# Kernel tuning notes

Measured on AMD Instinct MI355X. Metric: run time of the kernel, lower is better.

The kernel has to match this reference:

```python
import jax, jax.numpy as jnp
import numpy as np

BN_EPS = 1e-5

def binary_activation(x):
    # ReActNet BinaryActivation: forward = sign(x), backward = piecewise poly STE
    out_fwd = jnp.sign(x)
    m1 = (x < -1.0).astype(x.dtype)
    m2 = (x < 0.0).astype(x.dtype)
    m3 = (x < 1.0).astype(x.dtype)
    out1 = -1.0 * m1 + (x * x + 2.0 * x) * (1.0 - m1)
    out2 = out1 * m2 + (-x * x + 2.0 * x) * (1.0 - m2)
    out3 = out2 * m3 + 1.0 * (1.0 - m3)
    return jax.lax.stop_gradient(out_fwd - out3) + out3

def binary_conv3x3(x, w, stride=1):
    # per-output-channel scaling = mean |w| over (in, kh, kw), detached
    scale = jax.lax.stop_gradient(jnp.mean(jnp.abs(w), axis=(1, 2, 3), keepdims=True))
    bw_no_grad = jax.lax.stop_gradient(scale * jnp.sign(w))
    cw = jnp.clip(w, -1.0, 1.0)
    bw = bw_no_grad - jax.lax.stop_gradient(cw) + cw
    return jax.lax.conv_general_dilated(
        x, bw, window_strides=(stride, stride), padding=[(1, 1), (1, 1)],
        dimension_numbers=('NCHW', 'OIHW', 'NCHW'))

def batchnorm_inference(y, gamma, beta, mean, var):
    inv = gamma * jax.lax.rsqrt(var + BN_EPS)
    return y * inv[None, :, None, None] + (beta - mean * inv)[None, :, None, None]

def setup_inputs() -> dict:
    key = jax.random.key(0)
    k1, k2, k3 = jax.random.split(key, 3)
    N, Cin, Cout, H, W = 64, 128, 128, 56, 56
    x = jax.random.normal(k1, (N, Cin, H, W), dtype=jnp.float32)
    weight = jax.random.normal(k2, (Cout, Cin, 3, 3), dtype=jnp.float32) * 0.1
    gamma = jnp.ones((Cout,), dtype=jnp.float32)
    beta = jnp.zeros((Cout,), dtype=jnp.float32)
    bn_mean = jnp.zeros((Cout,), dtype=jnp.float32)
    bn_var = jax.random.uniform(k3, (Cout,), dtype=jnp.float32)
    return {"x": x, "weight": weight, "gamma": gamma, "beta": beta,
            "bn_mean": bn_mean, "bn_var": bn_var}

def reference(x, weight, gamma, beta, bn_mean, bn_var):
    residual = x
    out = binary_activation(x)
    out = binary_conv3x3(out, weight, stride=1)
    out = batchnorm_inference(out, gamma, beta, bn_mean, bn_var)
    return out + residual
```

## Files before the change

kernel.cpp:

```cpp
#include <hip/hip_runtime.h>


#define N_   64
#define C_   128
#define H_   56
#define W_   56
#define HW_  (H_*W_)
#define PH_  (H_+2)
#define PW_  (W_+2)
#define PHW_ (PH_*PW_)
#define NPIX (N_*HW_)
#define NPAD (N_*PHW_)
#define SBYTES ((size_t)NPAD * 128)
#define SPIX 264

typedef int v4i  __attribute__((ext_vector_type(4)));
typedef int v16i __attribute__((ext_vector_type(16)));

__device__ __forceinline__ void glds16(const char* g, char* l) {
    __builtin_amdgcn_global_load_lds(
        (const __attribute__((address_space(1))) void*)g,
        (__attribute__((address_space(3))) void*)l, 16, 0, 0);
}

__device__ __forceinline__ unsigned sign_byte(unsigned u) {
    return ((u << 1) == 0u) ? 0u : ((u >> 31) ? 0xFFu : 1u);
}

__global__ void prep_w_kernel(const float* __restrict__ w,
                              const float* __restrict__ gamma,
                              const float* __restrict__ beta,
                              const float* __restrict__ bn_mean,
                              const float* __restrict__ bn_var,
                              v4i* __restrict__ wfrag,
                              float2* __restrict__ AB) {
    const int o = blockIdx.x;
    const int lane = threadIdx.x;
    const float* wo = w + o * 1152;

    float s = 0.f;
    #pragma unroll
    for (int k = 0; k < 18; k++) s += fabsf(wo[k * 64 + lane]);
    #pragma unroll
    for (int off = 32; off > 0; off >>= 1) s += __shfl_down(s, off);

    #pragma unroll
    for (int rep = 0; rep < 2; rep++) {
        int f = rep * 64 + lane;
        if (f < 72) {
            int t = f >> 3, ks = (f >> 1) & 3, lh = f & 1;
            int cbase = ks * 32 + lh * 16;
            unsigned d[4];
            #pragma unroll
            for (int i = 0; i < 4; i++) {
                unsigned wd = 0;
                #pragma unroll
                for (int j = 0; j < 4; j++) {
                    unsigned u = __float_as_uint(wo[(cbase + i * 4 + j) * 9 + t]);
                    wd |= sign_byte(u) << (8 * j);
                }
                d[i] = wd;
            }
            v4i v; v.x=(int)d[0]; v.y=(int)d[1]; v.z=(int)d[2]; v.w=(int)d[3];
            wfrag[(((o >> 5) * 9 + t) * 4 + ks) * 64 + (lh << 5) + (o & 31)] = v;
        }
    }
    if (lane == 0) {
        float scale = s * (1.0f / 1152.0f);
        float inv = gamma[o] * rsqrtf(bn_var[o] + 1e-5f);
        float2 ab; ab.x = scale * inv; ab.y = beta[o] - bn_mean[o] * inv;
        AB[o] = ab;
    }
}

__global__ __launch_bounds__(256) void pack_s_kernel(
        const float* __restrict__ x, char* __restrict__ S) {
    const int tid = threadIdx.x;
    const int pixl = tid & 63, q = tid >> 6;
    const int b = blockIdx.x;

    if (b >= NPIX / 64) {
        int bt = (b - NPIX / 64) * 64 + pixl;
        int n = bt / 228, e = bt - n * 228;
        int ph, pw;
        if (e < 58)       { ph = 0;  pw = e; }
        else if (e < 116) { ph = 57; pw = e - 58; }
        else { int i = e - 116; ph = 1 + (i >> 1); pw = (i & 1) ? 57 : 0; }
        v4i z = {};
        char* dst = S + (size_t)((n * PH_ + ph) * PW_ + pw) * 128 + q * 32;
        ((v4i*)dst)[0] = z;
        ((v4i*)dst)[1] = z;
        return;
    }

    const int g = b * 64 + pixl;
    const int n = g / HW_;
    const int p = g - n * HW_;
    const int row = p / W_, col = p - row * W_;

    const float* xp = x + ((size_t)n * C_ + q * 32) * HW_ + p;
    unsigned w[8];
    #pragma unroll
    for (int i = 0; i < 8; i++) {
        unsigned wd = 0;
        #pragma unroll
        for (int j = 0; j < 4; j++) {
            unsigned u = __float_as_uint(xp[(i * 4 + j) * HW_]);
            wd |= sign_byte(u) << (8 * j);
        }
        w[i] = wd;
    }
    const int P = (n * PH_ + row + 1) * PW_ + col + 1;
    const int m = P & 7;
    char* base = S + (size_t)P * 128;
    v4i t0; t0.x=(int)w[0]; t0.y=(int)w[1]; t0.z=(int)w[2]; t0.w=(int)w[3];
    v4i t1; t1.x=(int)w[4]; t1.y=(int)w[5]; t1.z=(int)w[6]; t1.w=(int)w[7];
    *(v4i*)(base + (((2 * q)     ^ m) << 4)) = t0;
    *(v4i*)(base + (((2 * q + 1) ^ m) << 4)) = t1;
}

__global__ __launch_bounds__(256, 3) void bconv_mfma_kernel(
        const char* __restrict__ S,
        const v4i* __restrict__ wfrag,
        const float2* __restrict__ AB,
        const float* __restrict__ x,
        float* __restrict__ out) {
    __shared__ char Sl[SPIX * 128];

    const int tid = threadIdx.x;
    const int lane = tid & 63;
    const int wid = tid >> 6;
    const int l31 = lane & 31, lhi = lane >> 5;

    const int b0 = blockIdx.x;
    const int bid = (b0 & 7) * 200 + (b0 >> 3);
    const int n = bid / 25;
    const int pb = bid - n * 25;
    const int p0 = pb * 128;

    const int r0 = p0 / W_, c0 = p0 - r0 * W_;
    const int P0 = (n * PH_ + r0 + 1) * PW_ + (c0 + 1);
    const int qs8 = (P0 - PW_ - 1) & ~7;

    {
        const char* gsrc = S + (size_t)qs8 * 128 + lane * 16;
        #pragma unroll
        for (int i = 0; i < 9; i++) {
            int seg = i * 4 + wid;
            if (seg < (SPIX * 128) / 1024)
                glds16(gsrc + seg * 1024, &Sl[seg * 1024]);
        }
    }

    int lpx[4]; bool val[4]; int pix[4];
    #pragma unroll
    for (int ch = 0; ch < 4; ch++) {
        int p = p0 + ch * 32 + l31;
        val[ch] = (p < HW_);
        if (!val[ch]) p = HW_ - 1;
        pix[ch] = p;
        int r = p / W_, c = p - r * W_;
        lpx[ch] = (n * PH_ + r + 1) * PW_ + (c + 1) - qs8;
    }
    const int kc1 = lhi << 4;

    __syncthreads();

    v16i acc[4] = {};
    const v4i* wbase = wfrag + (size_t)wid * (9 * 4 * 64) + lane;

    v4i Acur[4], Anxt[4];
    #pragma unroll
    for (int ks = 0; ks < 4; ks++) Acur[ks] = wbase[ks * 64];

    #pragma unroll
    for (int t = 0; t < 9; t++) {
        if (t < 8) {
            #pragma unroll
            for (int ks = 0; ks < 4; ks++)
                Anxt[ks] = wbase[((t + 1) * 4 + ks) * 64];
        }
        const int tp = (t / 3 - 1) * PW_ + (t % 3 - 1);
        int A0[4];
        #pragma unroll
        for (int ch = 0; ch < 4; ch++) {
            int lpt = lpx[ch] + tp;
            A0[ch] = (lpt << 7) ^ ((lpt & 7) << 4) ^ kc1;
        }
        #pragma unroll
        for (int ks = 0; ks < 4; ks++) {
            #pragma unroll
            for (int ch = 0; ch < 4; ch++) {
                v4i bb = *(const v4i*)(&Sl[A0[ch] ^ (ks << 5)]);
                acc[ch] = __builtin_amdgcn_mfma_i32_32x32x32_i8(Acur[ks], bb,
                                                                acc[ch], 0, 0, 0);
            }
        }
        if (t < 8) {
            #pragma unroll
            for (int ks = 0; ks < 4; ks++) Acur[ks] = Anxt[ks];
        }
    }

    const int obase = wid * 32 + 4 * lhi;
    #pragma unroll
    for (int ch = 0; ch < 4; ch++) {
        if (!val[ch]) continue;
        unsigned base = (unsigned)n * (unsigned)(C_ * HW_) + (unsigned)pix[ch];
        #pragma unroll
        for (int r = 0; r < 16; r++) {
            int o = obase + (r & 3) + 8 * (r >> 2);
            float2 ab = AB[o];
            unsigned idx = base + (unsigned)o * (unsigned)HW_;
            out[idx] = fmaf(ab.x, (float)acc[ch][r], ab.y) + x[idx];
        }
    }
}

extern "C" void kernel_launch(void* const* d_in, const int* in_sizes, int n_in,
                              void* d_out, int out_size, void* d_ws, size_t ws_size,
                              hipStream_t stream) {
    const float* x      = (const float*)d_in[0];
    const float* weight = (const float*)d_in[1];
    const float* gamma  = (const float*)d_in[2];
    const float* beta   = (const float*)d_in[3];
    const float* bnmean = (const float*)d_in[4];
    const float* bnvar  = (const float*)d_in[5];
    float* out = (float*)d_out;

    char* ws = (char*)d_ws;
    char*   S     = ws;
    v4i*    wfrag = (v4i*)(ws + SBYTES);
    float2* AB    = (float2*)(ws + SBYTES + 147456);

    prep_w_kernel<<<128, 64, 0, stream>>>(weight, gamma, beta, bnmean, bnvar,
                                          wfrag, AB);
    pack_s_kernel<<<NPIX / 64 + 228, 256, 0, stream>>>(x, S);
    bconv_mfma_kernel<<<1600, 256, 0, stream>>>(S, wfrag, AB, x, out);
}
```

Measured before the change: 247.9 us.

## Tile conv over 8x8 spatial patches with 10x10 halo instead of row strips

The conv kernel now covers an 8x8 pixel tile per block, staging a 10x10 halo of packed sign bytes into LDS (13 KB instead of 33 KB). The XOR swizzle moves from the packing kernel into the LDS fill. Each wave computes two 32-pixel chunks instead of four, and the weight double-buffering is dropped. Launch bounds rise to allow 6 blocks per CU and the grid doubles to 3136 blocks. The aim is less redundant halo loading, higher occupancy and no wasted tail pixels, at the cost of less MFMA work per weight fragment load and more blocks.

```diff
diff --git a/kernel.cpp b/kernel.cpp
--- a/kernel.cpp
+++ b/kernel.cpp
@@ -12,7 +12,6 @@
 #define NPIX (N_*HW_)
 #define NPAD (N_*PHW_)
 #define SBYTES ((size_t)NPAD * 128)
-#define SPIX 264
 
 typedef int v4i  __attribute__((ext_vector_type(4)));
 typedef int v16i __attribute__((ext_vector_type(16)));
@@ -110,22 +109,20 @@
         }
         w[i] = wd;
     }
-    const int P = (n * PH_ + row + 1) * PW_ + col + 1;
-    const int m = P & 7;
-    char* base = S + (size_t)P * 128;
+    char* dst = S + (size_t)((n * PH_ + row + 1) * PW_ + col + 1) * 128 + q * 32;
     v4i t0; t0.x=(int)w[0]; t0.y=(int)w[1]; t0.z=(int)w[2]; t0.w=(int)w[3];
     v4i t1; t1.x=(int)w[4]; t1.y=(int)w[5]; t1.z=(int)w[6]; t1.w=(int)w[7];
-    *(v4i*)(base + (((2 * q)     ^ m) << 4)) = t0;
-    *(v4i*)(base + (((2 * q + 1) ^ m) << 4)) = t1;
-}
-
-__global__ __launch_bounds__(256, 3) void bconv_mfma_kernel(
+    ((v4i*)dst)[0] = t0;
+    ((v4i*)dst)[1] = t1;
+}
+
+__global__ __launch_bounds__(256, 6) void bconv_mfma_kernel(
         const char* __restrict__ S,
         const v4i* __restrict__ wfrag,
         const float2* __restrict__ AB,
         const float* __restrict__ x,
         float* __restrict__ out) {
-    __shared__ char Sl[SPIX * 128];
+    __shared__ char Sl[13312];
 
     const int tid = threadIdx.x;
     const int lane = tid & 63;
@@ -133,80 +130,66 @@
     const int l31 = lane & 31, lhi = lane >> 5;
 
     const int b0 = blockIdx.x;
-    const int bid = (b0 & 7) * 200 + (b0 >> 3);
-    const int n = bid / 25;
-    const int pb = bid - n * 25;
-    const int p0 = pb * 128;
-
-    const int r0 = p0 / W_, c0 = p0 - r0 * W_;
-    const int P0 = (n * PH_ + r0 + 1) * PW_ + (c0 + 1);
-    const int qs8 = (P0 - PW_ - 1) & ~7;
-
-    {
-        const char* gsrc = S + (size_t)qs8 * 128 + lane * 16;
-        #pragma unroll
-        for (int i = 0; i < 9; i++) {
-            int seg = i * 4 + wid;
-            if (seg < (SPIX * 128) / 1024)
-                glds16(gsrc + seg * 1024, &Sl[seg * 1024]);
-        }
-    }
-
-    int lpx[4]; bool val[4]; int pix[4];
-    #pragma unroll
-    for (int ch = 0; ch < 4; ch++) {
-        int p = p0 + ch * 32 + l31;
-        val[ch] = (p < HW_);
-        if (!val[ch]) p = HW_ - 1;
-        pix[ch] = p;
-        int r = p / W_, c = p - r * W_;
-        lpx[ch] = (n * PH_ + r + 1) * PW_ + (c + 1) - qs8;
-    }
-    const int kc1 = lhi << 4;
+    const int bid = (b0 & 7) * 392 + (b0 >> 3);
+    const int n = bid / 49;
+    const int pt = bid - n * 49;
+    const int pr = pt / 7, pc = pt - pr * 7;
+
+    const int Pw = (n * PH_ + pr * 8) * PW_ + pc * 8;
+
+    #pragma unroll
+    for (int j = 0; j < 13; j++) {
+        if ((j & 3) == wid) {
+            int chunk = j * 64 + lane;
+            int ck = chunk < 800 ? chunk : 799;
+            int wr = ck / 80;
+            int wc = ck - wr * 80;
+            int pxr = wc >> 3, s = wc & 7;
+            int px = wr * 10 + pxr;
+            const char* src = S + (size_t)(Pw + wr * PW_ + pxr) * 128
+                                + ((s ^ (px & 7)) << 4);
+            glds16(src, &Sl[j * 1024]);
+        }
+    }
+
+    const int lr = l31 >> 3, lc = l31 & 7;
+    int pxbase[2];
+    #pragma unroll
+    for (int ch = 0; ch < 2; ch++)
+        pxbase[ch] = (ch * 4 + lr) * 10 + lc;
 
     __syncthreads();
 
-    v16i acc[4] = {};
+    v16i acc[2] = {};
     const v4i* wbase = wfrag + (size_t)wid * (9 * 4 * 64) + lane;
 
-    v4i Acur[4], Anxt[4];
-    #pragma unroll
-    for (int ks = 0; ks < 4; ks++) Acur[ks] = wbase[ks * 64];
-
     #pragma unroll
     for (int t = 0; t < 9; t++) {
-        if (t < 8) {
-            #pragma unroll
-            for (int ks = 0; ks < 4; ks++)
-                Anxt[ks] = wbase[((t + 1) * 4 + ks) * 64];
-        }
-        const int tp = (t / 3 - 1) * PW_ + (t % 3 - 1);
-        int A0[4];
-        #pragma unroll
-        for (int ch = 0; ch < 4; ch++) {
-            int lpt = lpx[ch] + tp;
-            A0[ch] = (lpt << 7) ^ ((lpt & 7) << 4) ^ kc1;
-        }
+        const int toff = (t / 3) * 10 + (t % 3);
+        v4i a[4];
+        #pragma unroll
+        for (int ks = 0; ks < 4; ks++) a[ks] = wbase[(t * 4 + ks) * 64];
+        int px0 = pxbase[0] + toff;
+        int px1 = pxbase[1] + toff;
+        int A0 = (px0 << 7), k70 = (px0 & 7);
+        int A1 = (px1 << 7), k71 = (px1 & 7);
         #pragma unroll
         for (int ks = 0; ks < 4; ks++) {
-            #pragma unroll
-            for (int ch = 0; ch < 4; ch++) {
-                v4i bb = *(const v4i*)(&Sl[A0[ch] ^ (ks << 5)]);
-                acc[ch] = __builtin_amdgcn_mfma_i32_32x32x32_i8(Acur[ks], bb,
-                                                                acc[ch], 0, 0, 0);
-            }
-        }
-        if (t < 8) {
-            #pragma unroll
-            for (int ks = 0; ks < 4; ks++) Acur[ks] = Anxt[ks];
+            const int tslot = 2 * ks + lhi;
+            v4i b0 = *(const v4i*)(&Sl[A0 | ((tslot ^ k70) << 4)]);
+            v4i b1 = *(const v4i*)(&Sl[A1 | ((tslot ^ k71) << 4)]);
+            acc[0] = __builtin_amdgcn_mfma_i32_32x32x32_i8(a[ks], b0, acc[0], 0, 0, 0);
+            acc[1] = __builtin_amdgcn_mfma_i32_32x32x32_i8(a[ks], b1, acc[1], 0, 0, 0);
         }
     }
 
     const int obase = wid * 32 + 4 * lhi;
     #pragma unroll
-    for (int ch = 0; ch < 4; ch++) {
-        if (!val[ch]) continue;
-        unsigned base = (unsigned)n * (unsigned)(C_ * HW_) + (unsigned)pix[ch];
+    for (int ch = 0; ch < 2; ch++) {
+        int prow = pr * 8 + ch * 4 + lr;
+        int pcol = pc * 8 + lc;
+        unsigned base = (unsigned)n * (unsigned)(C_ * HW_)
+                      + (unsigned)(prow * W_ + pcol);
         #pragma unroll
         for (int r = 0; r < 16; r++) {
             int o = obase + (r & 3) + 8 * (r >> 2);
@@ -236,5 +219,5 @@
     prep_w_kernel<<<128, 64, 0, stream>>>(weight, gamma, beta, bnmean, bnvar,
                                           wfrag, AB);
     pack_s_kernel<<<NPIX / 64 + 228, 256, 0, stream>>>(x, S);
-    bconv_mfma_kernel<<<1600, 256, 0, stream>>>(S, wfrag, AB, x, out);
-}
+    bconv_mfma_kernel<<<3136, 256, 0, stream>>>(S, wfrag, AB, x, out);
+}
```

Result: slower. 271.5 us (+9.5%).
